# Optimization experiments

Measured on AMD Instinct MI355X. Metric: run time of the kernel, lower is better.

Reference implementation:

```python
import jax, jax.numpy as jnp
import numpy as np

EPS = 1e-5
INV_SQRT2 = 0.7071067811865476

def _rmsnorm(x, w):
    rms = jnp.sqrt(jnp.sum(x * x, axis=-1) / x.shape[-1] + EPS)
    return x / rms[..., None] * w

def _gelu(x):
    # exact erf-based GELU as in the torch module
    return x * (1.0 + jax.scipy.special.erf(x * INV_SQRT2)) * 0.5

def setup_inputs() -> dict:
    key = jax.random.key(0)
    ks = jax.random.split(key, 8)
    B, S, D, DFF = 4, 2048, 1024, 4096
    s = 0.02  # realistic init scale keeps softmax non-degenerate
    return {
        "x": jax.random.normal(ks[0], (B, S, D), jnp.float32),
        "ln1": jax.random.uniform(ks[1], (D,), jnp.float32),
        "ln2": jax.random.uniform(ks[2], (D,), jnp.float32),
        "ffn1": jax.random.normal(ks[3], (DFF, D), jnp.float32) * s,
        "ffn2": jax.random.normal(ks[4], (D, DFF), jnp.float32) * s,
        "k_proj": jax.random.normal(ks[5], (D, D), jnp.float32) * s,
        "q_proj": jax.random.normal(ks[6], (D, D), jnp.float32) * s,
        "v_proj": jax.random.normal(ks[7], (D, D), jnp.float32) * s,
        "out_proj": jax.random.normal(jax.random.fold_in(key, 99), (D, D), jnp.float32) * s,
    }

def reference(x, ln1, ln2, ffn1, ffn2, k_proj, q_proj, v_proj, out_proj):
    S = x.shape[1]
    d_k = x.shape[-1]
    # --- attention branch (single-head, as in source) ---
    h = _rmsnorm(x, ln1)
    Q = h @ q_proj.T  # [B,S,D]
    K = h @ k_proj.T
    V = h @ v_proj.T
    scores = jnp.einsum('bqd,bkd->bqk', Q, K) / jnp.sqrt(jnp.float32(d_k))
    attn = jax.nn.softmax(scores, axis=-1)
    # source: softmax first, then zero out strict-upper (future) entries, renormalize
    causal = jnp.tril(jnp.ones((S, S), jnp.float32))
    attn = attn * causal
    attn = attn / jnp.sum(attn, axis=-1, keepdims=True)
    mh = jnp.einsum('bqk,bkd->bqd', attn, V) @ out_proj
    y = x + mh
    # --- FFN branch: NOTE source feeds RMSNorm2(x), not y ---
    h2 = _rmsnorm(x, ln2)
    ff = _gelu(h2 @ ffn1.T) @ ffn2.T
    return y + ff
```

## Files before the change

### kernel.cpp

```cpp
#include <hip/hip_runtime.h>
#include <math.h>

typedef __bf16 bf16_t;
typedef __bf16 bf16x8 __attribute__((ext_vector_type(8)));
typedef float f32x4 __attribute__((ext_vector_type(4)));

#define LDS16(g, l) __builtin_amdgcn_global_load_lds( \
    (__attribute__((address_space(1))) void*)(g),     \
    (__attribute__((address_space(3))) void*)(l), 16, 0, 0)

__global__ __launch_bounds__(256) void prep_kernel(
    const float* __restrict__ qp, const float* __restrict__ kp,
    const float* __restrict__ vp, const float* __restrict__ f1,
    const float* __restrict__ f2, const float* __restrict__ op,
    const float* __restrict__ x, const float* __restrict__ ln1,
    bf16_t* __restrict__ qkvb, bf16_t* __restrict__ f1b,
    bf16_t* __restrict__ f2b, bf16_t* __restrict__ opT,
    bf16_t* __restrict__ h1)
{
    __shared__ float tile[32][33];
    __shared__ float red[4];
    int bid = blockIdx.x;
    int t = threadIdx.x;
    if (bid < 11264) {
        size_t i = ((size_t)bid * 256 + t) * 4;
        const float* src;
        bf16_t* dst;
        if (i < 3145728) {
            if (i < 1048576)      { src = qp + i;             dst = qkvb + i; }
            else if (i < 2097152) { src = kp + (i - 1048576); dst = qkvb + i; }
            else                  { src = vp + (i - 2097152); dst = qkvb + i; }
        } else if (i < 7340032) { src = f1 + (i - 3145728); dst = f1b + (i - 3145728); }
        else                    { src = f2 + (i - 7340032); dst = f2b + (i - 7340032); }
        float4 v = *(const float4*)src;
        dst[0] = (bf16_t)v.x; dst[1] = (bf16_t)v.y;
        dst[2] = (bf16_t)v.z; dst[3] = (bf16_t)v.w;
    } else if (bid < 12288) {
        int b2 = bid - 11264;
        int c0 = (b2 & 31) * 32, r0 = (b2 >> 5) * 32;
        int tx = t & 31, ty = t >> 5;
#pragma unroll
        for (int i = 0; i < 32; i += 8)
            tile[ty + i][tx] = op[(size_t)(r0 + ty + i) * 1024 + c0 + tx];
        __syncthreads();
#pragma unroll
        for (int i = 0; i < 32; i += 8)
            opT[(size_t)(c0 + ty + i) * 1024 + r0 + tx] = (bf16_t)tile[tx][ty + i];
    } else {
        int row = bid - 12288;
        float4 xv = ((const float4*)(x + (size_t)row * 1024))[t];
        float ss = xv.x * xv.x + xv.y * xv.y + xv.z * xv.z + xv.w * xv.w;
#pragma unroll
        for (int o = 32; o > 0; o >>= 1) ss += __shfl_xor(ss, o, 64);
        if ((t & 63) == 0) red[t >> 6] = ss;
        __syncthreads();
        ss = red[0] + red[1] + red[2] + red[3];
        float rinv = rsqrtf(ss * (1.0f / 1024.0f) + 1e-5f);
        float4 wv = ((const float4*)ln1)[t];
        bf16_t* hp = h1 + (size_t)row * 1024 + t * 4;
        hp[0] = (bf16_t)(xv.x * rinv * wv.x);
        hp[1] = (bf16_t)(xv.y * rinv * wv.y);
        hp[2] = (bf16_t)(xv.z * rinv * wv.z);
        hp[3] = (bf16_t)(xv.w * rinv * wv.w);
    }
}

__global__ __launch_bounds__(256) void rmsnorm_kernel(
    const float* __restrict__ x, const float* __restrict__ w,
    bf16_t* __restrict__ h)
{
    int row = blockIdx.x;
    int t = threadIdx.x;
    float4 xv = ((const float4*)(x + (size_t)row * 1024))[t];
    float ss = xv.x * xv.x + xv.y * xv.y + xv.z * xv.z + xv.w * xv.w;
#pragma unroll
    for (int o = 32; o > 0; o >>= 1) ss += __shfl_xor(ss, o, 64);
    __shared__ float red[4];
    if ((t & 63) == 0) red[t >> 6] = ss;
    __syncthreads();
    ss = red[0] + red[1] + red[2] + red[3];
    float rinv = rsqrtf(ss * (1.0f / 1024.0f) + 1e-5f);
    float4 wv = ((const float4*)w)[t];
    bf16_t* hp = h + (size_t)row * 1024 + t * 4;
    hp[0] = (bf16_t)(xv.x * rinv * wv.x);
    hp[1] = (bf16_t)(xv.y * rinv * wv.y);
    hp[2] = (bf16_t)(xv.z * rinv * wv.z);
    hp[3] = (bf16_t)(xv.w * rinv * wv.w);
}

__global__ __launch_bounds__(256) void transpose_bf16(
    const bf16_t* __restrict__ in, bf16_t* __restrict__ out,
    int rows, int ldin, long long sIn, long long sOut)
{
    __shared__ bf16_t tile[32][33];
    int b = blockIdx.z;
    const bf16_t* ip = in + (long long)b * sIn;
    bf16_t* op = out + (long long)b * sOut;
    int c0 = blockIdx.x * 32, r0 = blockIdx.y * 32;
    int tx = threadIdx.x & 31, ty = threadIdx.x >> 5;
#pragma unroll
    for (int i = 0; i < 32; i += 8)
        tile[ty + i][tx] = ip[(size_t)(r0 + ty + i) * ldin + c0 + tx];
    __syncthreads();
#pragma unroll
    for (int i = 0; i < 32; i += 8)
        op[(size_t)(c0 + ty + i) * rows + r0 + tx] = tile[tx][ty + i];
}

__global__ __launch_bounds__(256) void causal_softmax_kernel(bf16_t* __restrict__ SP)
{
    const int S = 2048;
    int q = blockIdx.x, b = blockIdx.y;
    bf16_t* row = SP + ((size_t)b * S + q) * S;
    int t = threadIdx.x;
    int j0 = t * 8;
    int Jstore = ((q >> 7) + 1) << 7;

    float v[8];
    if (j0 + 7 <= q) {
        bf16x8 xv = *(const bf16x8*)(row + j0);
#pragma unroll
        for (int i = 0; i < 8; i++) v[i] = (float)xv[i];
    } else if (j0 <= q) {
#pragma unroll
        for (int i = 0; i < 8; i++)
            v[i] = (j0 + i <= q) ? (float)row[j0 + i] : -1e30f;
    } else {
#pragma unroll
        for (int i = 0; i < 8; i++) v[i] = -1e30f;
    }

    float mx = v[0];
#pragma unroll
    for (int i = 1; i < 8; i++) mx = fmaxf(mx, v[i]);
#pragma unroll
    for (int o = 32; o > 0; o >>= 1) mx = fmaxf(mx, __shfl_xor(mx, o, 64));
    __shared__ float sm[4], ssum[4];
    if ((t & 63) == 0) sm[t >> 6] = mx;
    __syncthreads();
    mx = fmaxf(fmaxf(sm[0], sm[1]), fmaxf(sm[2], sm[3]));

    float e[8];
    float sum = 0.f;
#pragma unroll
    for (int i = 0; i < 8; i++) {
        e[i] = (v[i] > -1e29f) ? expf(v[i] - mx) : 0.f;
        sum += e[i];
    }
#pragma unroll
    for (int o = 32; o > 0; o >>= 1) sum += __shfl_xor(sum, o, 64);
    if ((t & 63) == 0) ssum[t >> 6] = sum;
    __syncthreads();
    sum = ssum[0] + ssum[1] + ssum[2] + ssum[3];
    float r = 1.0f / sum;

    if (j0 < Jstore) {
        bf16x8 ov;
#pragma unroll
        for (int i = 0; i < 8; i++) ov[i] = (bf16_t)(e[i] * r);
        *(bf16x8*)(row + j0) = ov;
    }
}

__global__ __launch_bounds__(256) void addp_kernel(
    float* __restrict__ out, const float* __restrict__ p1, int n4)
{
    int i = blockIdx.x * 256 + threadIdx.x;
    int stride = gridDim.x * 256;
    for (; i < n4; i += stride) {
        float4 a = ((const float4*)out)[i];
        float4 b = ((const float4*)p1)[i];
        a.x += b.x; a.y += b.y; a.z += b.z; a.w += b.w;
        ((float4*)out)[i] = a;
    }
}

template <int EPI, bool CSKIP, bool CKLOOP, bool ASPLIT>
__global__ __launch_bounds__(256) void gemm_bt(
    const bf16_t* __restrict__ A, const bf16_t* __restrict__ A2, int lda,
    const bf16_t* __restrict__ B, int ldb,
    void* Cv, int ldc, const float* R,
    int K, int Ksp, int Mt, long long sA, long long sB, long long sC,
    float scale)
{
    int id = blockIdx.x, bz = blockIdx.z;
    int xcd = id & 7, p = id >> 3;
    int chunk = Mt >> 3;
    int bm = xcd * chunk + (p % chunk);
    int bn = p / chunk;
    if (CSKIP && bn > bm) return;

    __shared__ __align__(16) bf16_t At[128 * 64];
    __shared__ __align__(16) bf16_t Bt[128 * 64];
    int t = threadIdx.x;
    int w = t >> 6, l = t & 63;
    int wm = w >> 1, wn = w & 1;
    int lane_m = l & 15, quad = l >> 4;

    const bf16_t* Ag = A + (long long)bz * sA + (size_t)(bm * 128) * lda;
    const bf16_t* Bg = B + (long long)bz * sB + (size_t)(bn * 128) * ldb;

    int Keff = K;
    if (CKLOOP) {
        int kk = (bm + 1) * 128;
        if (kk < K) Keff = kk;
    }

    f32x4 acc[4][4] = {};

    int rb = w * 8 + (l >> 3);
    int g0 = ((l & 7) ^ ((l >> 3) & 7)) * 8;
    const bf16_t* a0[4];
    const bf16_t* a1[4];
    const bf16_t* b0[4];
#pragma unroll
    for (int j = 0; j < 4; j++) {
        size_t ro = (size_t)(rb + 32 * j);
        a0[j] = Ag + ro * lda + g0;
        if (ASPLIT) a1[j] = A2 + (long long)bz * sA + (size_t)(bm * 128) * lda
                           + ro * lda + g0;
        b0[j] = Bg + ro * ldb + g0;
    }

    int s0 = (quad ^ (lane_m & 7)) * 8;
    int s1 = ((4 + quad) ^ (lane_m & 7)) * 8;

    for (int kt = 0; kt < Keff; kt += 64) {
        __syncthreads();
#pragma unroll
        for (int j = 0; j < 4; j++) {
            const bf16_t* pa = a0[j] + kt;
            if (ASPLIT && kt >= Ksp) pa = a1[j] + (kt - Ksp);
            LDS16(pa, At + (size_t)w * 512 + j * 2048);
            LDS16(b0[j] + kt, Bt + (size_t)w * 512 + j * 2048);
        }
        __syncthreads();

#pragma unroll
        for (int h = 0; h < 2; h++) {
            int sh = h ? s1 : s0;
            bf16x8 af[4], bfr[4];
#pragma unroll
            for (int mi = 0; mi < 4; mi++)
                af[mi] = *(const bf16x8*)(At + (wm * 64 + mi * 16 + lane_m) * 64 + sh);
#pragma unroll
            for (int ni = 0; ni < 4; ni++)
                bfr[ni] = *(const bf16x8*)(Bt + (wn * 64 + ni * 16 + lane_m) * 64 + sh);
#pragma unroll
            for (int mi = 0; mi < 4; mi++)
#pragma unroll
                for (int ni = 0; ni < 4; ni++)
                    acc[mi][ni] = __builtin_amdgcn_mfma_f32_16x16x32_bf16(
                        af[mi], bfr[ni], acc[mi][ni], 0, 0, 0);
        }
    }

    long long cbase = (long long)bz * sC;
#pragma unroll
    for (int mi = 0; mi < 4; mi++) {
#pragma unroll
        for (int r = 0; r < 4; r++) {
            int row = bm * 128 + wm * 64 + mi * 16 + quad * 4 + r;
#pragma unroll
            for (int ni = 0; ni < 4; ni++) {
                int col = bn * 128 + wn * 64 + ni * 16 + lane_m;
                float v = acc[mi][ni][r];
                size_t idx = (size_t)(cbase + (long long)row * ldc + col);
                if (EPI == 0) {
                    ((bf16_t*)Cv)[idx] = (bf16_t)(v * scale);
                } else if (EPI == 1) {
                    float g = 0.5f * v * (1.0f + erff(v * 0.70710678118654752f));
                    ((bf16_t*)Cv)[idx] = (bf16_t)g;
                } else {
                    float rv = R[(size_t)row * ldc + col];
                    ((float*)Cv)[idx] = v + rv;
                }
            }
        }
    }
}

#define VM8 asm volatile("s_waitcnt vmcnt(8)" ::: "memory")
#define VM4 asm volatile("s_waitcnt vmcnt(4)" ::: "memory")
#define VM0 asm volatile("s_waitcnt vmcnt(0)" ::: "memory")
#define NOP ((void)0)

#define STAGE_A(BUF, KH, KOFF) do { \
    LDS16(rA0 + (KOFF), &As[BUF][KH][w * 512]);        \
    LDS16(rA1 + (KOFF), &As[BUF][KH][4096 + w * 512]); } while (0)
#define STAGE_B(BUF, KH, KOFF) do { \
    LDS16(rB0 + (KOFF), &Bs[BUF][KH][w * 512]);        \
    LDS16(rB1 + (KOFF), &Bs[BUF][KH][4096 + w * 512]); } while (0)

#define PHASE(BUF, KH, MQ, STAGE_STMT, WAIT_STMT)                             \
  {                                                                           \
    _Pragma("unroll") for (int mi = 0; mi < 4; mi++)                          \
        af[mi] = *(const bf16x8*)&As[BUF][KH][arow + (MQ)*2048 + mi*512];     \
    if ((MQ) == 0) {                                                          \
      _Pragma("unroll") for (int ni = 0; ni < 4; ni++)                        \
          bfr[ni] = *(const bf16x8*)&Bs[BUF][KH][brow + ni*512];              \
    }                                                                         \
    STAGE_STMT;                                                               \
    __builtin_amdgcn_s_barrier();                                             \
    asm volatile("s_waitcnt lgkmcnt(0)" ::: "memory");                        \
    __builtin_amdgcn_sched_barrier(0);                                        \
    __builtin_amdgcn_s_setprio(1);                                            \
    _Pragma("unroll") for (int mi = 0; mi < 4; mi++)                          \
      _Pragma("unroll") for (int ni = 0; ni < 4; ni++)                        \
        acc[(MQ)*4 + mi][ni] = __builtin_amdgcn_mfma_f32_16x16x32_bf16(       \
            af[mi], bfr[ni], acc[(MQ)*4 + mi][ni], 0, 0, 0);                  \
    __builtin_amdgcn_s_setprio(0);                                            \
    WAIT_STMT;                                                                \
    __builtin_amdgcn_s_barrier();                                             \
  }

template <int EPI>
__global__ __launch_bounds__(512, 2) void gemm256(
    const bf16_t* __restrict__ A, int lda,
    const bf16_t* __restrict__ B, int ldb,
    void* Cv, int ldc, const float* R, float* C2, int Ksp,
    int K, int Nt, float scale)
{
    int id = blockIdx.x;
    int xcd = id & 7, p = id >> 3;
    int chunk = gridDim.x >> 3;
    int g = xcd * chunk + p;
    int bm = g / Nt, bn = g % Nt;
    int sK = (EPI == 3) ? blockIdx.y : 0;

    __shared__ __align__(16) bf16_t As[2][2][256 * 32];
    __shared__ __align__(16) bf16_t Bs[2][2][256 * 32];

    int t = threadIdx.x;
    int w = t >> 6, l = t & 63;
    int wm = w >> 2, wn = w & 3;
    int lm = l & 15, quad = l >> 4;

    const bf16_t* Ag = A + (size_t)(bm * 256) * lda + (size_t)sK * Ksp;
    const bf16_t* Bg = B + (size_t)(bn * 256) * ldb + (size_t)sK * Ksp;

    int g4 = ((l & 3) ^ ((l >> 3) & 3)) * 8;
    const bf16_t* rA0 = Ag + (size_t)(w * 16 + (l >> 2)) * lda + g4;
    const bf16_t* rA1 = rA0 + (size_t)128 * lda;
    const bf16_t* rB0 = Bg + (size_t)(w * 16 + (l >> 2)) * ldb + g4;
    const bf16_t* rB1 = rB0 + (size_t)128 * ldb;

    int slot8 = (quad ^ ((lm >> 1) & 3)) * 8;
    int arow = (wm * 128 + lm) * 32 + slot8;
    int brow = (wn * 64 + lm) * 32 + slot8;

    f32x4 acc[8][4] = {};
    bf16x8 af[4], bfr[4];

    STAGE_A(0, 0, 0);  STAGE_B(0, 0, 0);
    STAGE_A(0, 1, 32); STAGE_B(0, 1, 32);
    STAGE_A(1, 0, 64); STAGE_B(1, 0, 64);
    VM8;
    __builtin_amdgcn_s_barrier();

    int T = K >> 7;
    for (int it = 0; it < T - 1; ++it) {
        int kb = it << 7;
        PHASE(0, 0, 0, STAGE_A(1, 1, kb + 96),  NOP);
        PHASE(0, 0, 1, STAGE_B(1, 1, kb + 96),  VM8);
        PHASE(0, 1, 0, STAGE_A(0, 0, kb + 128), NOP);
        PHASE(0, 1, 1, STAGE_B(0, 0, kb + 128), VM8);
        PHASE(1, 0, 0, STAGE_A(0, 1, kb + 160), NOP);
        PHASE(1, 0, 1, STAGE_B(0, 1, kb + 160), VM8);
        PHASE(1, 1, 0, STAGE_A(1, 0, kb + 192), NOP);
        PHASE(1, 1, 1, STAGE_B(1, 0, kb + 192), VM8);
    }
    {
        int kb = (T - 1) << 7;
        PHASE(0, 0, 0, STAGE_A(1, 1, kb + 96), NOP);
        PHASE(0, 0, 1, STAGE_B(1, 1, kb + 96), VM8);
        PHASE(0, 1, 0, NOP, NOP);
        PHASE(0, 1, 1, NOP, VM4);
        PHASE(1, 0, 0, NOP, NOP);
        PHASE(1, 0, 1, NOP, VM0);
        PHASE(1, 1, 0, NOP, NOP);
        PHASE(1, 1, 1, NOP, NOP);
    }

#pragma unroll
    for (int mq = 0; mq < 2; mq++) {
#pragma unroll
        for (int mi = 0; mi < 4; mi++) {
#pragma unroll
            for (int r = 0; r < 4; r++) {
                int row = bm * 256 + wm * 128 + mq * 64 + mi * 16 + quad * 4 + r;
#pragma unroll
                for (int ni = 0; ni < 4; ni++) {
                    int col = bn * 256 + wn * 64 + ni * 16 + lm;
                    float v = acc[mq * 4 + mi][ni][r];
                    size_t idx = (size_t)row * ldc + col;
                    if (EPI == 0) {
                        ((bf16_t*)Cv)[idx] = (bf16_t)(v * scale);
                    } else if (EPI == 1) {
                        float ge = 0.5f * v * (1.0f + erff(v * 0.70710678118654752f));
                        ((bf16_t*)Cv)[idx] = (bf16_t)ge;
                    } else if (EPI == 2) {
                        float rv = R[(size_t)row * ldc + col];
                        ((float*)Cv)[idx] = v + rv;
                    } else {
                        if (sK == 0) {
                            float rv = R[(size_t)row * ldc + col];
                            ((float*)Cv)[idx] = v + rv;
                        } else {
                            C2[idx] = v;
                        }
                    }
                }
            }
        }
    }
}

extern "C" void kernel_launch(void* const* d_in, const int* in_sizes, int n_in,
                              void* d_out, int out_size, void* d_ws, size_t ws_size,
                              hipStream_t stream)
{
    (void)in_sizes; (void)n_in; (void)out_size;
    const float* x    = (const float*)d_in[0];
    const float* ln1  = (const float*)d_in[1];
    const float* ln2  = (const float*)d_in[2];
    const float* ffn1 = (const float*)d_in[3];
    const float* ffn2 = (const float*)d_in[4];
    const float* kp   = (const float*)d_in[5];
    const float* qp   = (const float*)d_in[6];
    const float* vp   = (const float*)d_in[7];
    const float* op   = (const float*)d_in[8];
    float* out = (float*)d_out;

    const size_t MiB = 1048576;
    char* ws = (char*)d_ws;
    bf16_t* qkvb = (bf16_t*)(ws + 0 * MiB);
    bf16_t* opT  = (bf16_t*)(ws + 6 * MiB);
    bf16_t* f1b  = (bf16_t*)(ws + 8 * MiB);
    bf16_t* f2b  = (bf16_t*)(ws + 16 * MiB);
    bf16_t* h1   = (bf16_t*)(ws + 24 * MiB);
    bf16_t* VT   = (bf16_t*)(ws + 24 * MiB);
    bf16_t* h2   = (bf16_t*)(ws + 24 * MiB);
    bf16_t* QKVb = (bf16_t*)(ws + 40 * MiB);
    bf16_t* AV   = (bf16_t*)(ws + 40 * MiB);
    bf16_t* G0   = (bf16_t*)(ws + 40 * MiB);
    float*  P1   = (float*)(ws + 104 * MiB);
    bf16_t* SP   = (bf16_t*)d_out;
    bool bigws  = ws_size >= 104 * MiB;
    bool splitw = ws_size >= 136 * MiB;

    dim3 blk(256);
    dim3 blk5(512);
    const int HUGE_K = 1 << 30;

    prep_kernel<<<dim3(20480), blk, 0, stream>>>(
        qp, kp, vp, ffn1, ffn2, op, x, ln1, qkvb, f1b, f2b, opT, h1);

    gemm256<0><<<dim3(384), blk5, 0, stream>>>(
        h1, 1024, qkvb, 1024, QKVb, 3072, nullptr, nullptr, 0, 1024, 12, 1.0f);

    gemm_bt<0, true, false, false><<<dim3(256, 1, 4), blk, 0, stream>>>(
        QKVb, QKVb, 3072, QKVb + 1024, 3072, SP, 2048, nullptr,
        1024, HUGE_K, 16,
        (long long)2048 * 3072, (long long)2048 * 3072, (long long)2048 * 2048,
        1.0f / 32.0f);

    transpose_bf16<<<dim3(32, 64, 4), blk, 0, stream>>>(
        QKVb + 2048, VT, 2048, 3072,
        (long long)2048 * 3072, (long long)1024 * 2048);

    causal_softmax_kernel<<<dim3(2048, 4), blk, 0, stream>>>(SP);

    gemm_bt<0, false, true, false><<<dim3(128, 1, 4), blk, 0, stream>>>(
        SP, SP, 2048, VT, 2048, AV, 1024, nullptr,
        2048, HUGE_K, 16,
        (long long)2048 * 2048, (long long)1024 * 2048, (long long)2048 * 1024,
        1.0f);

    gemm256<2><<<dim3(128), blk5, 0, stream>>>(
        AV, 1024, opT, 1024, out, 1024, x, nullptr, 0, 1024, 4, 1.0f);

    rmsnorm_kernel<<<dim3(8192), blk, 0, stream>>>(x, ln2, h2);

    if (bigws) {
        gemm256<1><<<dim3(512), blk5, 0, stream>>>(
            h2, 1024, f1b, 1024, G0, 4096, nullptr, nullptr, 0, 1024, 16, 1.0f);
        if (splitw) {
            gemm256<3><<<dim3(128, 2), blk5, 0, stream>>>(
                G0, 4096, f2b, 4096, out, 1024, out, P1, 2048, 2048, 4, 1.0f);
            addp_kernel<<<dim3(2048), blk, 0, stream>>>(out, P1, 2097152);
        } else {
            gemm256<2><<<dim3(128), blk5, 0, stream>>>(
                G0, 4096, f2b, 4096, out, 1024, out, nullptr, 0, 4096, 4, 1.0f);
        }
    } else {
        for (int half = 0; half < 2; half++) {
            gemm_bt<1, false, false, false><<<dim3(1024), blk, 0, stream>>>(
                h2, h2, 1024, f1b + (size_t)half * 2048 * 1024, 1024, G0, 2048,
                nullptr, 1024, HUGE_K, 64, 0, 0, 0, 1.0f);
            gemm_bt<2, false, false, false><<<dim3(512), blk, 0, stream>>>(
                G0, G0, 2048, f2b + half * 2048, 4096, out, 1024, out,
                2048, HUGE_K, 64, 0, 0, 0, 1.0f);
        }
    }
}
```

Baseline: 554.2 us.

## Double-buffer LDS fragment registers to overlap ds_reads with MFMA in gemm256

New measurement: 585.1 us. 5.6% more time.

```diff
diff --git a/kernel.cpp b/kernel.cpp
--- a/kernel.cpp
+++ b/kernel.cpp
@@ -280,7 +280,7 @@
     }
 }
 
-#define VM8 asm volatile("s_waitcnt vmcnt(8)" ::: "memory")
+#define VM6 asm volatile("s_waitcnt vmcnt(6)" ::: "memory")
 #define VM4 asm volatile("s_waitcnt vmcnt(4)" ::: "memory")
 #define VM0 asm volatile("s_waitcnt vmcnt(0)" ::: "memory")
 #define NOP ((void)0)
@@ -292,25 +292,30 @@
     LDS16(rB0 + (KOFF), &Bs[BUF][KH][w * 512]);        \
     LDS16(rB1 + (KOFF), &Bs[BUF][KH][4096 + w * 512]); } while (0)
 
-#define PHASE(BUF, KH, MQ, STAGE_STMT, WAIT_STMT)                             \
+#define RD_A(DST, BUF, KH, MQ) do {                                     \
+    DST[0] = *(const bf16x8*)&As[BUF][KH][arow + (MQ)*2048 + 0*512];    \
+    DST[1] = *(const bf16x8*)&As[BUF][KH][arow + (MQ)*2048 + 1*512];    \
+    DST[2] = *(const bf16x8*)&As[BUF][KH][arow + (MQ)*2048 + 2*512];    \
+    DST[3] = *(const bf16x8*)&As[BUF][KH][arow + (MQ)*2048 + 3*512]; } while (0)
+#define RD_B(DST, BUF, KH) do {                                         \
+    DST[0] = *(const bf16x8*)&Bs[BUF][KH][brow + 0*512];                \
+    DST[1] = *(const bf16x8*)&Bs[BUF][KH][brow + 1*512];                \
+    DST[2] = *(const bf16x8*)&Bs[BUF][KH][brow + 2*512];                \
+    DST[3] = *(const bf16x8*)&Bs[BUF][KH][brow + 3*512]; } while (0)
+
+#define PHASE(AFC, BFC, MQ, NRD_STMT, LGK, STAGE_STMT, VMW_STMT)              \
   {                                                                           \
-    _Pragma("unroll") for (int mi = 0; mi < 4; mi++)                          \
-        af[mi] = *(const bf16x8*)&As[BUF][KH][arow + (MQ)*2048 + mi*512];     \
-    if ((MQ) == 0) {                                                          \
-      _Pragma("unroll") for (int ni = 0; ni < 4; ni++)                        \
-          bfr[ni] = *(const bf16x8*)&Bs[BUF][KH][brow + ni*512];              \
-    }                                                                         \
+    NRD_STMT;                                                                 \
     STAGE_STMT;                                                               \
-    __builtin_amdgcn_s_barrier();                                             \
-    asm volatile("s_waitcnt lgkmcnt(0)" ::: "memory");                        \
+    asm volatile("s_waitcnt lgkmcnt(" #LGK ")" ::: "memory");                 \
     __builtin_amdgcn_sched_barrier(0);                                        \
     __builtin_amdgcn_s_setprio(1);                                            \
     _Pragma("unroll") for (int mi = 0; mi < 4; mi++)                          \
       _Pragma("unroll") for (int ni = 0; ni < 4; ni++)                        \
         acc[(MQ)*4 + mi][ni] = __builtin_amdgcn_mfma_f32_16x16x32_bf16(       \
-            af[mi], bfr[ni], acc[(MQ)*4 + mi][ni], 0, 0, 0);                  \
+            AFC[mi], BFC[ni], acc[(MQ)*4 + mi][ni], 0, 0, 0);                 \
     __builtin_amdgcn_s_setprio(0);                                            \
-    WAIT_STMT;                                                                \
+    VMW_STMT;                                                                 \
     __builtin_amdgcn_s_barrier();                                             \
   }
 
@@ -350,36 +355,54 @@
     int brow = (wn * 64 + lm) * 32 + slot8;
 
     f32x4 acc[8][4] = {};
-    bf16x8 af[4], bfr[4];
+    bf16x8 af0[4], af1[4], bfr0[4], bfr1[4];
 
     STAGE_A(0, 0, 0);  STAGE_B(0, 0, 0);
     STAGE_A(0, 1, 32); STAGE_B(0, 1, 32);
     STAGE_A(1, 0, 64); STAGE_B(1, 0, 64);
-    VM8;
+    asm volatile("s_waitcnt vmcnt(8)" ::: "memory");
     __builtin_amdgcn_s_barrier();
+    RD_A(af0, 0, 0, 0);
+    RD_B(bfr0, 0, 0);
 
     int T = K >> 7;
     for (int it = 0; it < T - 1; ++it) {
         int kb = it << 7;
-        PHASE(0, 0, 0, STAGE_A(1, 1, kb + 96),  NOP);
-        PHASE(0, 0, 1, STAGE_B(1, 1, kb + 96),  VM8);
-        PHASE(0, 1, 0, STAGE_A(0, 0, kb + 128), NOP);
-        PHASE(0, 1, 1, STAGE_B(0, 0, kb + 128), VM8);
-        PHASE(1, 0, 0, STAGE_A(0, 1, kb + 160), NOP);
-        PHASE(1, 0, 1, STAGE_B(0, 1, kb + 160), VM8);
-        PHASE(1, 1, 0, STAGE_A(1, 0, kb + 192), NOP);
-        PHASE(1, 1, 1, STAGE_B(1, 0, kb + 192), VM8);
+        PHASE(af0, bfr0, 0, RD_A(af1, 0, 0, 1),                      4,
+              STAGE_A(1, 1, kb + 96), VM6);
+        PHASE(af1, bfr0, 1, { RD_A(af0, 0, 1, 0); RD_B(bfr1, 0, 1); }, 8,
+              STAGE_B(1, 1, kb + 96), NOP);
+        PHASE(af0, bfr1, 0, RD_A(af1, 0, 1, 1),                      4,
+              STAGE_A(0, 0, kb + 128), VM6);
+        PHASE(af1, bfr1, 1, { RD_A(af0, 1, 0, 0); RD_B(bfr0, 1, 0); }, 8,
+              STAGE_B(0, 0, kb + 128), NOP);
+        PHASE(af0, bfr0, 0, RD_A(af1, 1, 0, 1),                      4,
+              STAGE_A(0, 1, kb + 160), VM6);
+        PHASE(af1, bfr0, 1, { RD_A(af0, 1, 1, 0); RD_B(bfr1, 1, 1); }, 8,
+              STAGE_B(0, 1, kb + 160), NOP);
+        PHASE(af0, bfr1, 0, RD_A(af1, 1, 1, 1),                      4,
+              STAGE_A(1, 0, kb + 192), VM6);
+        PHASE(af1, bfr1, 1, { RD_A(af0, 0, 0, 0); RD_B(bfr0, 0, 0); }, 8,
+              STAGE_B(1, 0, kb + 192), NOP);
     }
     {
         int kb = (T - 1) << 7;
-        PHASE(0, 0, 0, STAGE_A(1, 1, kb + 96), NOP);
-        PHASE(0, 0, 1, STAGE_B(1, 1, kb + 96), VM8);
-        PHASE(0, 1, 0, NOP, NOP);
-        PHASE(0, 1, 1, NOP, VM4);
-        PHASE(1, 0, 0, NOP, NOP);
-        PHASE(1, 0, 1, NOP, VM0);
-        PHASE(1, 1, 0, NOP, NOP);
-        PHASE(1, 1, 1, NOP, NOP);
+        PHASE(af0, bfr0, 0, RD_A(af1, 0, 0, 1),                      4,
+              STAGE_A(1, 1, kb + 96), VM6);
+        PHASE(af1, bfr0, 1, { RD_A(af0, 0, 1, 0); RD_B(bfr1, 0, 1); }, 8,
+              STAGE_B(1, 1, kb + 96), NOP);
+        PHASE(af0, bfr1, 0, RD_A(af1, 0, 1, 1),                      4,
+              NOP, VM4);
+        PHASE(af1, bfr1, 1, { RD_A(af0, 1, 0, 0); RD_B(bfr0, 1, 0); }, 8,
+              NOP, NOP);
+        PHASE(af0, bfr0, 0, RD_A(af1, 1, 0, 1),                      4,
+              NOP, VM0);
+        PHASE(af1, bfr0, 1, { RD_A(af0, 1, 1, 0); RD_B(bfr1, 1, 1); }, 8,
+              NOP, NOP);
+        PHASE(af0, bfr1, 0, RD_A(af1, 1, 1, 1),                      4,
+              NOP, NOP);
+        PHASE(af1, bfr1, 1, NOP,                                     0,
+              NOP, NOP);
     }
 
 #pragma unroll
```
